# Optimization experiments

Measured on AMD Instinct MI355X. Metric: run time of the kernel, lower is better.

The kernel has to match this reference:

```python
import jax, jax.numpy as jnp
import numpy as np

B, T, I, H = 256, 512, 300, 128


def setup_inputs() -> dict:
    key = jax.random.key(0)
    ks = jax.random.split(key, 7)
    s_ih = 1.0 / np.sqrt(H)
    return {
        "x": jax.random.normal(ks[0], (B, T, I), dtype=jnp.float32),
        # PyTorch LSTM params, gate order i,f,g,o stacked along first axis
        "W_ih": jax.random.uniform(ks[1], (4 * H, I), minval=-s_ih, maxval=s_ih, dtype=jnp.float32),
        "W_hh": jax.random.uniform(ks[2], (4 * H, H), minval=-s_ih, maxval=s_ih, dtype=jnp.float32),
        "b_ih": jax.random.uniform(ks[3], (4 * H,), minval=-s_ih, maxval=s_ih, dtype=jnp.float32),
        "b_hh": jax.random.uniform(ks[4], (4 * H,), minval=-s_ih, maxval=s_ih, dtype=jnp.float32),
        "fc_w": jax.random.uniform(ks[5], (1, H), minval=-s_ih, maxval=s_ih, dtype=jnp.float32),
        "fc_b": jax.random.uniform(ks[6], (1,), minval=-s_ih, maxval=s_ih, dtype=jnp.float32),
    }


def _lstm_last_h(x, W_ih, W_hh, b_ih, b_hh):
    # Precompute input contributions for all timesteps at once: [B,T,4H]
    xg = jnp.einsum("bti,gi->btg", x, W_ih) + b_ih + b_hh
    xg = jnp.transpose(xg, (1, 0, 2))  # [T,B,4H] for scan

    def step(carry, xg_t):
        h, c = carry
        gates = xg_t + h @ W_hh.T  # [B,4H]
        i, f, g, o = jnp.split(gates, 4, axis=-1)
        i = jax.nn.sigmoid(i)
        f = jax.nn.sigmoid(f)
        g = jnp.tanh(g)
        o = jax.nn.sigmoid(o)
        c = f * c + i * g
        h = o * jnp.tanh(c)
        return (h, c), None

    h0 = jnp.zeros((x.shape[0], W_hh.shape[1]), dtype=x.dtype)
    (h_last, _), _ = jax.lax.scan(step, (h0, h0), xg)
    return h_last  # [B,H]


def reference(x, W_ih, W_hh, b_ih, b_hh, fc_w, fc_b):
    h_last = _lstm_last_h(x, W_ih, W_hh, b_ih, b_hh)
    return h_last @ fc_w.T + fc_b  # [B,1]
```

## Files before the change

kernel.cpp:

```cpp
#include <hip/hip_runtime.h>
#include <cstdint>
#include <cstddef>

#define Bb   256
#define Tt   512
#define Ii   300
#define Hh   128
#define G4   512
#define KP   320
#define Mm   (Bb*Tt)

typedef _Float16 h2v   __attribute__((ext_vector_type(2)));
typedef _Float16 half8 __attribute__((ext_vector_type(8)));
typedef float    f32x4 __attribute__((ext_vector_type(4)));

static __device__ __forceinline__ h2v as_h2(unsigned int u){ union{unsigned int u; h2v h;} c; c.u=u; return c.h; }
static __device__ __forceinline__ unsigned int as_u32(h2v h){ union{unsigned int u; h2v h;} c; c.h=h; return c.u; }

#if __has_builtin(__builtin_amdgcn_fdot2)
#define FDOT2(a,b,c) __builtin_amdgcn_fdot2((a),(b),(c),false)
#else
static __device__ __forceinline__ float FDOT2(h2v a, h2v b, float c){
  return c + (float)a[0]*(float)b[0] + (float)a[1]*(float)b[1];
}
#endif

__global__ __launch_bounds__(256) void conv_x(const float* __restrict__ x, unsigned int* __restrict__ x16){
  int idx = blockIdx.x*256 + threadIdx.x;
  int r   = idx / 160;
  int kk2 = idx - r*160;
  int kk  = kk2*2;
  const float* xr = x + (size_t)r*Ii;
  float v0 = (kk   < Ii) ? xr[kk]   : 0.f;
  float v1 = (kk+1 < Ii) ? xr[kk+1] : 0.f;
  h2v h; h[0] = (_Float16)v0; h[1] = (_Float16)v1;
  x16[idx] = as_u32(h);
}

__global__ __launch_bounds__(256) void conv_small(const float* __restrict__ Wih, const float* __restrict__ Whh,
      const float* __restrict__ bih, const float* __restrict__ bhh,
      unsigned int* __restrict__ W16, unsigned int* __restrict__ Whh2, float* __restrict__ bias){
  int idx = blockIdx.x*256 + threadIdx.x;
  if (idx < G4*160){
    int pr = idx/160, kk2 = idx - pr*160, kk = kk2*2;
    int gc = (pr&3)*128 + (pr>>2);
    const float* wr = Wih + (size_t)gc*Ii;
    float v0 = (kk   < Ii) ? wr[kk]   : 0.f;
    float v1 = (kk+1 < Ii) ? wr[kk+1] : 0.f;
    h2v h; h[0]=(_Float16)v0; h[1]=(_Float16)v1;
    W16[idx] = as_u32(h);
  } else if (idx < G4*160 + G4*64){
    int t = idx - G4*160; int pr = t>>6, kk = t&63;
    int gc = (pr&3)*128 + (pr>>2);
    float v0 = Whh[gc*Hh + kk*2], v1 = Whh[gc*Hh + kk*2 + 1];
    h2v h; h[0]=(_Float16)v0; h[1]=(_Float16)v1;
    Whh2[t] = as_u32(h);
  } else if (idx < G4*160 + G4*64 + G4){
    int pr = idx - (G4*160 + G4*64);
    int gc = (pr&3)*128 + (pr>>2);
    bias[pr] = bih[gc] + bhh[gc];
  }
}

__global__ __launch_bounds__(256,2) void gemm16(const _Float16* __restrict__ A, const _Float16* __restrict__ Bm,
       const float* __restrict__ bias, float* __restrict__ C){
  __shared__ _Float16 As[128][32];
  __shared__ _Float16 Bs[128][32];
  int tid = threadIdx.x;
  int w = tid>>6, lane = tid&63;
  int bm = blockIdx.x*128, bn = blockIdx.y*128;
  f32x4 acc[2][8];
  #pragma unroll
  for (int i=0;i<2;i++)
    #pragma unroll
    for (int j=0;j<8;j++) acc[i][j] = (f32x4){0.f,0.f,0.f,0.f};

  int srow = tid>>1, scol = (tid&1)*16;
  const uint4* ga = (const uint4*)(A  + (size_t)(bm+srow)*KP + scol);
  const uint4* gb = (const uint4*)(Bm + (size_t)(bn+srow)*KP + scol);

  int q = lane>>4, mr = lane&15;
  int m0 = w*32;

  for (int kt=0; kt<KP/32; ++kt){
    __syncthreads();
    uint4 va0 = ga[0], va1 = ga[1];
    uint4 vb0 = gb[0], vb1 = gb[1];
    *(uint4*)&As[srow][scol]   = va0; *(uint4*)&As[srow][scol+8] = va1;
    *(uint4*)&Bs[srow][scol]   = vb0; *(uint4*)&Bs[srow][scol+8] = vb1;
    ga += 4; gb += 4;
    __syncthreads();
    half8 af0 = *(const half8*)&As[m0 + mr][q*8];
    half8 af1 = *(const half8*)&As[m0 + 16 + mr][q*8];
    #pragma unroll
    for (int j=0;j<8;j++){
      half8 bf = *(const half8*)&Bs[j*16 + mr][q*8];
      acc[0][j] = __builtin_amdgcn_mfma_f32_16x16x32_f16(af0, bf, acc[0][j], 0,0,0);
      acc[1][j] = __builtin_amdgcn_mfma_f32_16x16x32_f16(af1, bf, acc[1][j], 0,0,0);
    }
  }
  #pragma unroll
  for (int j=0;j<8;j++){
    int gc = bn + j*16 + mr;
    float bv = bias[gc];
    #pragma unroll
    for (int i=0;i<2;i++){
      int gr0 = bm + w*32 + i*16 + q*4;
      #pragma unroll
      for (int reg=0; reg<4; ++reg)
        C[(size_t)(gr0+reg)*G4 + gc] = acc[i][j][reg] + bv;
    }
  }
}

__global__ __launch_bounds__(512,1) void lstm_rec(const float* __restrict__ xg, const unsigned int* __restrict__ Whh2,
     const float* __restrict__ fcw, const float* __restrict__ fcb, float* __restrict__ out){
  int tid = threadIdx.x;
  int b = blockIdx.x;
  int d = tid >> 2, g = tid & 3;
  h2v w[64];
  #pragma unroll
  for (int kk=0; kk<64; ++kk) w[kk] = as_h2(Whh2[tid*64 + kk]);

  __shared__ __align__(16) unsigned short hsh[2][128];
  __shared__ float red[128];
  if (tid < 128) hsh[0][tid] = 0;
  float creg = 0.f, hreg = 0.f;
  const float* xrow = xg + (size_t)b * (Tt*G4);
  float xc = xrow[tid];
  int b0 = g & 1;
  int b1 = (g >> 1) & 1;
  float km = (g == 2) ? 2.f : 1.f;
  __syncthreads();

  for (int t=0; t<Tt; ++t){
    float xn = 0.f;
    if (t < Tt-1) xn = xrow[(size_t)(t+1)*G4 + tid];
    const uint4* hv = (const uint4*)hsh[t & 1];
    float a0 = xc, a1 = 0.f, a2 = 0.f, a3 = 0.f;
    #pragma unroll
    for (int kq=0; kq<8; ++kq){
      uint4 hq0 = hv[kq*2], hq1 = hv[kq*2+1];
      a0 = FDOT2(as_h2(hq0.x), w[kq*8+0], a0); a1 = FDOT2(as_h2(hq0.y), w[kq*8+1], a1);
      a2 = FDOT2(as_h2(hq0.z), w[kq*8+2], a2); a3 = FDOT2(as_h2(hq0.w), w[kq*8+3], a3);
      a0 = FDOT2(as_h2(hq1.x), w[kq*8+4], a0); a1 = FDOT2(as_h2(hq1.y), w[kq*8+5], a1);
      a2 = FDOT2(as_h2(hq1.z), w[kq*8+6], a2); a3 = FDOT2(as_h2(hq1.w), w[kq*8+7], a3);
    }
    float a = (a0 + a1) + (a2 + a3);
    float s  = 1.f/(1.f + __expf(-km*a));
    float act = (g == 2) ? (2.f*s - 1.f) : s;
    float u1 = __shfl_xor(act, 1);
    float u2 = __shfl_xor(act, 2);
    float u3 = __shfl_xor(act, 3);
    float pl = b0 ? u1  : act;
    float ph = b0 ? u3  : u2;
    float ql = b0 ? act : u1;
    float qh = b0 ? u2  : u3;
    float i_ = b1 ? ph : pl;
    float f_ = b1 ? qh : ql;
    float g_ = b1 ? pl : ph;
    float o_ = b1 ? ql : qh;
    creg = f_*creg + i_*g_;
    float ec = __expf(2.f*creg); float tc = 1.f - 2.f/(ec+1.f);
    hreg = o_*tc;
    if (g == 0){
      union{ _Float16 f; unsigned short s; } cv; cv.f = (_Float16)hreg;
      hsh[(t+1) & 1][d] = cv.s;
    }
    __syncthreads();
    xc = xn;
  }

  if (g == 0) red[d] = hreg * fcw[d];
  __syncthreads();
  #pragma unroll
  for (int s2=64; s2>=1; s2>>=1){
    if (tid < s2) red[tid] += red[tid+s2];
    __syncthreads();
  }
  if (tid == 0) out[b] = red[0] + fcb[0];
}

extern "C" void kernel_launch(void* const* d_in, const int* in_sizes, int n_in,
                              void* d_out, int out_size, void* d_ws, size_t ws_size,
                              hipStream_t stream){
  const float* x   = (const float*)d_in[0];
  const float* Wih = (const float*)d_in[1];
  const float* Whh = (const float*)d_in[2];
  const float* bih = (const float*)d_in[3];
  const float* bhh = (const float*)d_in[4];
  const float* fcw = (const float*)d_in[5];
  const float* fcb = (const float*)d_in[6];
  float* out = (float*)d_out;
  char* ws = (char*)d_ws;

  unsigned int* x16   = (unsigned int*)(ws);
  unsigned int* W16   = (unsigned int*)(ws + 83886080);
  unsigned int* Whh2w = (unsigned int*)(ws + 84213760);
  float*        bias  = (float*)      (ws + 84344832);
  float*        xg    = (float*)      (ws + 84346880);

  hipLaunchKernelGGL(conv_x,     dim3(81920),  dim3(256), 0, stream, x, x16);
  hipLaunchKernelGGL(conv_small, dim3(450),    dim3(256), 0, stream, Wih, Whh, bih, bhh, W16, Whh2w, bias);
  hipLaunchKernelGGL(gemm16,     dim3(1024,4), dim3(256), 0, stream,
                     (const _Float16*)x16, (const _Float16*)W16, bias, xg);
  hipLaunchKernelGGL(lstm_rec,   dim3(256),    dim3(512), 0, stream, xg, Whh2w, fcw, fcb, out);
}
```

Before: 638.9 us.

## Fuse input projection GEMM into LSTM recurrence with producer warps

Removes the separate x conversion and input-projection GEMM kernels. The recurrent kernel now runs 1024 threads per block: 512 threads keep the existing recurrence, and the other 512 act as producers. The producers convert chunks of 16 timesteps of x to fp16 in LDS, compute their gate projections with MFMA and write them into a double-buffered LDS ring. This avoids writing and re-reading the large xg intermediate through global memory and overlaps the projection with the serial recurrence. The cost is heavier LDS use (about 74KB), only one block per CU on 256 CUs, and a W_ih re-read from global/L2 per chunk.

```diff
diff --git a/kernel.cpp b/kernel.cpp
--- a/kernel.cpp
+++ b/kernel.cpp
@@ -8,7 +8,8 @@
 #define Hh   128
 #define G4   512
 #define KP   320
-#define Mm   (Bb*Tt)
+#define CH   16
+#define NCH  (Tt/CH)
 
 typedef _Float16 h2v   __attribute__((ext_vector_type(2)));
 typedef _Float16 half8 __attribute__((ext_vector_type(8)));
@@ -24,18 +25,6 @@
   return c + (float)a[0]*(float)b[0] + (float)a[1]*(float)b[1];
 }
 #endif
-
-__global__ __launch_bounds__(256) void conv_x(const float* __restrict__ x, unsigned int* __restrict__ x16){
-  int idx = blockIdx.x*256 + threadIdx.x;
-  int r   = idx / 160;
-  int kk2 = idx - r*160;
-  int kk  = kk2*2;
-  const float* xr = x + (size_t)r*Ii;
-  float v0 = (kk   < Ii) ? xr[kk]   : 0.f;
-  float v1 = (kk+1 < Ii) ? xr[kk+1] : 0.f;
-  h2v h; h[0] = (_Float16)v0; h[1] = (_Float16)v1;
-  x16[idx] = as_u32(h);
-}
 
 __global__ __launch_bounds__(256) void conv_small(const float* __restrict__ Wih, const float* __restrict__ Whh,
       const float* __restrict__ bih, const float* __restrict__ bhh,
@@ -62,116 +51,140 @@
   }
 }
 
-__global__ __launch_bounds__(256,2) void gemm16(const _Float16* __restrict__ A, const _Float16* __restrict__ Bm,
-       const float* __restrict__ bias, float* __restrict__ C){
-  __shared__ _Float16 As[128][32];
-  __shared__ _Float16 Bs[128][32];
-  int tid = threadIdx.x;
-  int w = tid>>6, lane = tid&63;
-  int bm = blockIdx.x*128, bn = blockIdx.y*128;
-  f32x4 acc[2][8];
-  #pragma unroll
-  for (int i=0;i<2;i++)
-    #pragma unroll
-    for (int j=0;j<8;j++) acc[i][j] = (f32x4){0.f,0.f,0.f,0.f};
-
-  int srow = tid>>1, scol = (tid&1)*16;
-  const uint4* ga = (const uint4*)(A  + (size_t)(bm+srow)*KP + scol);
-  const uint4* gb = (const uint4*)(Bm + (size_t)(bn+srow)*KP + scol);
-
-  int q = lane>>4, mr = lane&15;
-  int m0 = w*32;
-
-  for (int kt=0; kt<KP/32; ++kt){
-    __syncthreads();
-    uint4 va0 = ga[0], va1 = ga[1];
-    uint4 vb0 = gb[0], vb1 = gb[1];
-    *(uint4*)&As[srow][scol]   = va0; *(uint4*)&As[srow][scol+8] = va1;
-    *(uint4*)&Bs[srow][scol]   = vb0; *(uint4*)&Bs[srow][scol+8] = vb1;
-    ga += 4; gb += 4;
-    __syncthreads();
-    half8 af0 = *(const half8*)&As[m0 + mr][q*8];
-    half8 af1 = *(const half8*)&As[m0 + 16 + mr][q*8];
-    #pragma unroll
-    for (int j=0;j<8;j++){
-      half8 bf = *(const half8*)&Bs[j*16 + mr][q*8];
-      acc[0][j] = __builtin_amdgcn_mfma_f32_16x16x32_f16(af0, bf, acc[0][j], 0,0,0);
-      acc[1][j] = __builtin_amdgcn_mfma_f32_16x16x32_f16(af1, bf, acc[1][j], 0,0,0);
-    }
-  }
-  #pragma unroll
-  for (int j=0;j<8;j++){
-    int gc = bn + j*16 + mr;
-    float bv = bias[gc];
-    #pragma unroll
-    for (int i=0;i<2;i++){
-      int gr0 = bm + w*32 + i*16 + q*4;
-      #pragma unroll
-      for (int reg=0; reg<4; ++reg)
-        C[(size_t)(gr0+reg)*G4 + gc] = acc[i][j][reg] + bv;
-    }
-  }
-}
-
-__global__ __launch_bounds__(512,1) void lstm_rec(const float* __restrict__ xg, const unsigned int* __restrict__ Whh2,
+__global__ __launch_bounds__(1024,1) void lstm_fused(const float* __restrict__ x,
+     const _Float16* __restrict__ Wih16, const float* __restrict__ bias,
+     const unsigned int* __restrict__ Whh2,
      const float* __restrict__ fcw, const float* __restrict__ fcb, float* __restrict__ out){
   int tid = threadIdx.x;
   int b = blockIdx.x;
-  int d = tid >> 2, g = tid & 3;
-  h2v w[64];
-  #pragma unroll
-  for (int kk=0; kk<64; ++kk) w[kk] = as_h2(Whh2[tid*64 + kk]);
-
+
+  __shared__ float ring[2][CH*G4];
+  __shared__ __align__(16) _Float16 Axl[CH][KP];
   __shared__ __align__(16) unsigned short hsh[2][128];
   __shared__ float red[128];
-  if (tid < 128) hsh[0][tid] = 0;
+
+  int d = tid >> 2, g = tid & 3;
+  int b0 = g & 1, b1 = (g >> 1) & 1;
+  float km = (g == 2) ? 2.f : 1.f;
+  h2v w[64];
   float creg = 0.f, hreg = 0.f;
-  const float* xrow = xg + (size_t)b * (Tt*G4);
-  float xc = xrow[tid];
-  int b0 = g & 1;
-  int b1 = (g >> 1) & 1;
-  float km = (g == 2) ? 2.f : 1.f;
+
+  int pw  = (tid >> 6) - 8;
+  int pln = tid & 63;
+  int pq = pln >> 4, pmr = pln & 15;
+  f32x4 acc[4];
+  float biasv[4];
+  #pragma unroll
+  for (int j=0;j<4;j++) acc[j] = (f32x4){0.f,0.f,0.f,0.f};
+
+  auto stage_x = [&](int c){
+    #pragma unroll
+    for (int i=0;i<2;i++){
+      int idx = (tid - 512) + i*512;
+      if (idx < CH*40){
+        int r = idx/40, k = idx - r*40;
+        union{ _Float16 h[8]; uint4 u; } o;
+        const float* src = x + (size_t)(b*Tt + c*CH + r)*Ii + k*8;
+        if (k < 37){
+          float4 a4 = *(const float4*)src;
+          float4 c4 = *(const float4*)(src+4);
+          o.h[0]=(_Float16)a4.x; o.h[1]=(_Float16)a4.y; o.h[2]=(_Float16)a4.z; o.h[3]=(_Float16)a4.w;
+          o.h[4]=(_Float16)c4.x; o.h[5]=(_Float16)c4.y; o.h[6]=(_Float16)c4.z; o.h[7]=(_Float16)c4.w;
+        } else if (k == 37){
+          float4 a4 = *(const float4*)src;
+          o.h[0]=(_Float16)a4.x; o.h[1]=(_Float16)a4.y; o.h[2]=(_Float16)a4.z; o.h[3]=(_Float16)a4.w;
+          o.h[4]=(_Float16)0.f; o.h[5]=(_Float16)0.f; o.h[6]=(_Float16)0.f; o.h[7]=(_Float16)0.f;
+        } else {
+          o.u = (uint4){0u,0u,0u,0u};
+        }
+        *(uint4*)&Axl[r][k*8] = o.u;
+      }
+    }
+  };
+  auto produce_kt = [&](int kt){
+    const _Float16* wb = Wih16 + (size_t)(pw*64 + pmr)*KP + kt*32 + pq*8;
+    half8 bf0 = *(const half8*)(wb);
+    half8 bf1 = *(const half8*)(wb + (size_t)16*KP);
+    half8 bf2 = *(const half8*)(wb + (size_t)32*KP);
+    half8 bf3 = *(const half8*)(wb + (size_t)48*KP);
+    half8 af  = *(const half8*)&Axl[pmr][kt*32 + pq*8];
+    acc[0] = __builtin_amdgcn_mfma_f32_16x16x32_f16(af, bf0, acc[0], 0,0,0);
+    acc[1] = __builtin_amdgcn_mfma_f32_16x16x32_f16(af, bf1, acc[1], 0,0,0);
+    acc[2] = __builtin_amdgcn_mfma_f32_16x16x32_f16(af, bf2, acc[2], 0,0,0);
+    acc[3] = __builtin_amdgcn_mfma_f32_16x16x32_f16(af, bf3, acc[3], 0,0,0);
+  };
+  auto write_ring = [&](int bw){
+    #pragma unroll
+    for (int j=0;j<4;j++){
+      int gate = pw*64 + j*16 + pmr;
+      #pragma unroll
+      for (int rg=0;rg<4;rg++)
+        ring[bw][(pq*4+rg)*G4 + gate] = acc[j][rg] + biasv[j];
+      acc[j] = (f32x4){0.f,0.f,0.f,0.f};
+    }
+  };
+
+  if (tid < 512){
+    #pragma unroll
+    for (int kk=0; kk<64; ++kk) w[kk] = as_h2(Whh2[tid*64 + kk]);
+    if (tid < 128) hsh[0][tid] = 0;
+  } else {
+    #pragma unroll
+    for (int j=0;j<4;j++) biasv[j] = bias[pw*64 + j*16 + pmr];
+    stage_x(0);
+  }
   __syncthreads();
+  if (tid >= 512){
+    #pragma unroll
+    for (int kt=0; kt<KP/32; ++kt) produce_kt(kt);
+    write_ring(0);
+  }
+  __syncthreads();
 
   for (int t=0; t<Tt; ++t){
-    float xn = 0.f;
-    if (t < Tt-1) xn = xrow[(size_t)(t+1)*G4 + tid];
-    const uint4* hv = (const uint4*)hsh[t & 1];
-    float a0 = xc, a1 = 0.f, a2 = 0.f, a3 = 0.f;
-    #pragma unroll
-    for (int kq=0; kq<8; ++kq){
-      uint4 hq0 = hv[kq*2], hq1 = hv[kq*2+1];
-      a0 = FDOT2(as_h2(hq0.x), w[kq*8+0], a0); a1 = FDOT2(as_h2(hq0.y), w[kq*8+1], a1);
-      a2 = FDOT2(as_h2(hq0.z), w[kq*8+2], a2); a3 = FDOT2(as_h2(hq0.w), w[kq*8+3], a3);
-      a0 = FDOT2(as_h2(hq1.x), w[kq*8+4], a0); a1 = FDOT2(as_h2(hq1.y), w[kq*8+5], a1);
-      a2 = FDOT2(as_h2(hq1.z), w[kq*8+6], a2); a3 = FDOT2(as_h2(hq1.w), w[kq*8+7], a3);
-    }
-    float a = (a0 + a1) + (a2 + a3);
-    float s  = 1.f/(1.f + __expf(-km*a));
-    float act = (g == 2) ? (2.f*s - 1.f) : s;
-    float u1 = __shfl_xor(act, 1);
-    float u2 = __shfl_xor(act, 2);
-    float u3 = __shfl_xor(act, 3);
-    float pl = b0 ? u1  : act;
-    float ph = b0 ? u3  : u2;
-    float ql = b0 ? act : u1;
-    float qh = b0 ? u2  : u3;
-    float i_ = b1 ? ph : pl;
-    float f_ = b1 ? qh : ql;
-    float g_ = b1 ? pl : ph;
-    float o_ = b1 ? ql : qh;
-    creg = f_*creg + i_*g_;
-    float ec = __expf(2.f*creg); float tc = 1.f - 2.f/(ec+1.f);
-    hreg = o_*tc;
-    if (g == 0){
-      union{ _Float16 f; unsigned short s; } cv; cv.f = (_Float16)hreg;
-      hsh[(t+1) & 1][d] = cv.s;
+    if (tid < 512){
+      float xc = ring[(t>>4)&1][(t&15)*G4 + tid];
+      const uint4* hv = (const uint4*)hsh[t & 1];
+      float a0 = xc, a1 = 0.f, a2 = 0.f, a3 = 0.f;
+      #pragma unroll
+      for (int kq=0; kq<8; ++kq){
+        uint4 hq0 = hv[kq*2], hq1 = hv[kq*2+1];
+        a0 = FDOT2(as_h2(hq0.x), w[kq*8+0], a0); a1 = FDOT2(as_h2(hq0.y), w[kq*8+1], a1);
+        a2 = FDOT2(as_h2(hq0.z), w[kq*8+2], a2); a3 = FDOT2(as_h2(hq0.w), w[kq*8+3], a3);
+        a0 = FDOT2(as_h2(hq1.x), w[kq*8+4], a0); a1 = FDOT2(as_h2(hq1.y), w[kq*8+5], a1);
+        a2 = FDOT2(as_h2(hq1.z), w[kq*8+6], a2); a3 = FDOT2(as_h2(hq1.w), w[kq*8+7], a3);
+      }
+      float a = (a0 + a1) + (a2 + a3);
+      float s_  = 1.f/(1.f + __expf(-km*a));
+      float act = (g == 2) ? (2.f*s_ - 1.f) : s_;
+      float u1 = __shfl_xor(act, 1);
+      float u2 = __shfl_xor(act, 2);
+      float u3 = __shfl_xor(act, 3);
+      float pl = b0 ? u1  : act;
+      float ph = b0 ? u3  : u2;
+      float ql = b0 ? act : u1;
+      float qh = b0 ? u2  : u3;
+      float i_ = b1 ? ph : pl;
+      float f_ = b1 ? qh : ql;
+      float g_ = b1 ? pl : ph;
+      float o_ = b1 ? ql : qh;
+      creg = f_*creg + i_*g_;
+      float ec = __expf(2.f*creg); float tc = 1.f - 2.f/(ec+1.f);
+      hreg = o_*tc;
+      if (g == 0){
+        union{ _Float16 f; unsigned short s; } cv; cv.f = (_Float16)hreg;
+        hsh[(t+1) & 1][d] = cv.s;
+      }
+    } else if (t < Tt - CH){
+      int s = t & 15;
+      if (s == 0)                stage_x((t>>4) + 1);
+      else if (s >= 2 && s < 12) produce_kt(s - 2);
+      else if (s == 12)          write_ring(((t>>4) + 1) & 1);
     }
     __syncthreads();
-    xc = xn;
-  }
-
-  if (g == 0) red[d] = hreg * fcw[d];
+  }
+
+  if (tid < 512 && g == 0) red[d] = hreg * fcw[d];
   __syncthreads();
   #pragma unroll
   for (int s2=64; s2>=1; s2>>=1){
@@ -194,15 +207,11 @@
   float* out = (float*)d_out;
   char* ws = (char*)d_ws;
 
-  unsigned int* x16   = (unsigned int*)(ws);
   unsigned int* W16   = (unsigned int*)(ws + 83886080);
   unsigned int* Whh2w = (unsigned int*)(ws + 84213760);
   float*        bias  = (float*)      (ws + 84344832);
-  float*        xg    = (float*)      (ws + 84346880);
-
-  hipLaunchKernelGGL(conv_x,     dim3(81920),  dim3(256), 0, stream, x, x16);
-  hipLaunchKernelGGL(conv_small, dim3(450),    dim3(256), 0, stream, Wih, Whh, bih, bhh, W16, Whh2w, bias);
-  hipLaunchKernelGGL(gemm16,     dim3(1024,4), dim3(256), 0, stream,
-                     (const _Float16*)x16, (const _Float16*)W16, bias, xg);
-  hipLaunchKernelGGL(lstm_rec,   dim3(256),    dim3(512), 0, stream, xg, Whh2w, fcw, fcb, out);
-}
+
+  hipLaunchKernelGGL(conv_small, dim3(450), dim3(256), 0, stream, Wih, Whh, bih, bhh, W16, Whh2w, bias);
+  hipLaunchKernelGGL(lstm_fused, dim3(256), dim3(1024), 0, stream,
+                     x, (const _Float16*)W16, bias, Whh2w, fcw, fcb, out);
+}
```

New measurement: 759.1 us. 1.19x slower.
